# Kernel tuning notes

Hardware: AMD Instinct MI355X
Metric: run time of the kernel (lower is better)

Reference implementation:

```python
import jax, jax.numpy as jnp
import numpy as np

D_ENC = 640  # encoder feature dim


def setup_inputs() -> dict:
    key = jax.random.key(0)
    k1, k2, k3 = jax.random.split(key, 3)
    B, T, U1 = 8, 256, 65  # U1 = maxU + 1
    D_pred = 640
    V = 1024  # num_outputs + 1
    encoder_out = jax.random.normal(k1, (B, T, D_ENC), dtype=jnp.float32)
    predictor_out = jax.random.normal(k2, (B, U1, D_pred), dtype=jnp.float32)
    W = jax.random.normal(k3, (D_ENC + D_pred, V), dtype=jnp.float32) * 0.02
    b = jnp.zeros((V,), dtype=jnp.float32)
    return {"encoder_out": encoder_out, "predictor_out": predictor_out, "W": W, "b": b}


def reference(encoder_out, predictor_out, W, b):
    # Original: tile enc over U+1, tile pred over T, concat on feature dim, Dense.
    # Mathematically identical: split W into encoder/predictor halves and
    # broadcast-add the two projections (avoids the O(T*U*2D) concat buffer).
    We = W[:D_ENC]   # [D_enc, V]
    Wp = W[D_ENC:]   # [D_pred, V]
    enc_proj = jnp.einsum("btd,dv->btv", encoder_out, We)      # [B, T, V]
    pred_proj = jnp.einsum("bud,dv->buv", predictor_out, Wp)   # [B, U+1, V]
    out = enc_proj[:, :, None, :] + pred_proj[:, None, :, :] + b  # [B, T, U+1, V]
    return out
```

## Files before the change

kernel.cpp:

```cpp
#include <hip/hip_runtime.h>

constexpr int B  = 8;
constexpr int T  = 256;
constexpr int U1 = 65;
constexpr int DK = 640;
constexpr int V  = 1024;

constexpr int M_ENC  = B * T;
constexpr int M_PRED = B * U1;

constexpr int NKS  = DK / 32;
constexpr int RT_E = M_ENC / 16;
constexpr int RT_P = 36;
constexpr int CT   = V / 16;

typedef float  f32x4  __attribute__((ext_vector_type(4)));
typedef short  short8 __attribute__((ext_vector_type(8)));
typedef unsigned short u16x4 __attribute__((ext_vector_type(4)));

__device__ __forceinline__ short f2bf(float f) {
    union { float f; unsigned u; } x; x.f = f;
    unsigned r = x.u + 0x7fffu + ((x.u >> 16) & 1u);
    return (short)(r >> 16);
}
__device__ __forceinline__ f32x4 bf4_to_f32(u16x4 s) {
    f32x4 o;
    union { unsigned u; float f; } x;
    x.u = ((unsigned)s[0]) << 16; o[0] = x.f;
    x.u = ((unsigned)s[1]) << 16; o[1] = x.f;
    x.u = ((unsigned)s[2]) << 16; o[2] = x.f;
    x.u = ((unsigned)s[3]) << 16; o[3] = x.f;
    return o;
}

constexpr int NB_AE = RT_E * NKS * 64 / 256;
constexpr int NB_AP = RT_P * NKS * 64 / 256;
constexpr int NB_BE = CT   * NKS * 64 / 256;
constexpr int NB_BP = NB_BE;

__global__ __launch_bounds__(256) void prep_kernel(
    const float* __restrict__ enc, const float* __restrict__ pred,
    const float* __restrict__ W,
    short* __restrict__ Apack_e, short* __restrict__ Apack_p,
    short* __restrict__ Bpack_e, short* __restrict__ Bpack_p)
{
    const int bid = blockIdx.x;
    const int tid = threadIdx.x;

    if (bid < NB_AE) {
        const int chunk = bid * 256 + tid;
        const int l  = chunk & 63;
        const int ks = (chunk >> 6) % NKS;
        const int rt = chunk / (64 * NKS);
        const int row = rt * 16 + (l & 15);
        const float* src = enc + (size_t)row * DK + ks * 32 + (l >> 4) * 8;
        const f32x4 x = *reinterpret_cast<const f32x4*>(src);
        const f32x4 y = *reinterpret_cast<const f32x4*>(src + 4);
        short8 s;
        s[0]=f2bf(x[0]); s[1]=f2bf(x[1]); s[2]=f2bf(x[2]); s[3]=f2bf(x[3]);
        s[4]=f2bf(y[0]); s[5]=f2bf(y[1]); s[6]=f2bf(y[2]); s[7]=f2bf(y[3]);
        *reinterpret_cast<short8*>(Apack_e + (size_t)chunk * 8) = s;
    } else if (bid < NB_AE + NB_AP) {
        const int chunk = (bid - NB_AE) * 256 + tid;
        const int l  = chunk & 63;
        const int ks = (chunk >> 6) % NKS;
        const int rt = chunk / (64 * NKS);
        const int row = rt * 16 + (l & 15);
        short8 s;
        if (row < M_PRED) {
            const float* src = pred + (size_t)row * DK + ks * 32 + (l >> 4) * 8;
            const f32x4 x = *reinterpret_cast<const f32x4*>(src);
            const f32x4 y = *reinterpret_cast<const f32x4*>(src + 4);
            s[0]=f2bf(x[0]); s[1]=f2bf(x[1]); s[2]=f2bf(x[2]); s[3]=f2bf(x[3]);
            s[4]=f2bf(y[0]); s[5]=f2bf(y[1]); s[6]=f2bf(y[2]); s[7]=f2bf(y[3]);
        } else {
            #pragma unroll
            for (int j = 0; j < 8; ++j) s[j] = 0;
        }
        *reinterpret_cast<short8*>(Apack_p + (size_t)chunk * 8) = s;
    } else {
        const bool isE = (bid < NB_AE + NB_AP + NB_BE);
        const int  base = isE ? (NB_AE + NB_AP) : (NB_AE + NB_AP + NB_BE);
        short* Bp = isE ? Bpack_e : Bpack_p;
        const int kofs = isE ? 0 : DK;
        const int chunk = (bid - base) * 256 + tid;
        const int l  = chunk & 63;
        const int ks = (chunk >> 6) % NKS;
        const int ct = chunk / (64 * NKS);
        const int v  = ct * 16 + (l & 15);
        const int k0 = kofs + ks * 32 + (l >> 4) * 8;
        short8 s;
        #pragma unroll
        for (int j = 0; j < 8; ++j)
            s[j] = f2bf(W[(size_t)(k0 + j) * V + v]);
        *reinterpret_cast<short8*>(Bp + (size_t)chunk * 8) = s;
    }
}

constexpr int NB_GE = (M_ENC / 64) * 16;
constexpr int NB_GP = (RT_P / 4) * 16;

__global__ __launch_bounds__(256) void gemm_kernel(
    const short* __restrict__ Apack_e, const short* __restrict__ Apack_p,
    const short* __restrict__ Bpack_e, const short* __restrict__ Bpack_p,
    const float* __restrict__ bias,
    short* __restrict__ enc_proj, short* __restrict__ pred_proj)
{
    const bool isE = (blockIdx.x < NB_GE);
    const int  lb  = isE ? blockIdx.x : blockIdx.x - NB_GE;
    const int  rb  = lb >> 4;
    const int  cb  = lb & 15;

    const short* Ap = isE ? Apack_e : Apack_p;
    const short* Bp = isE ? Bpack_e : Bpack_p;
    short* O        = isE ? enc_proj : pred_proj;
    const int M     = isE ? M_ENC : M_PRED;

    const int wid  = threadIdx.x >> 6;
    const int lane = threadIdx.x & 63;
    const int wr   = wid >> 1, wc = wid & 1;
    const int m    = lane & 15, g = lane >> 4;

    const int rt0 = rb * 4 + wr * 2;
    const int ct0 = cb * 4 + wc * 2;

    const short* a0p = Ap + ((size_t)rt0 * NKS) * 512 + lane * 8;
    const short* a1p = a0p + (size_t)NKS * 512;
    const short* b0p = Bp + ((size_t)ct0 * NKS) * 512 + lane * 8;
    const short* b1p = b0p + (size_t)NKS * 512;

    f32x4 z4; z4[0]=z4[1]=z4[2]=z4[3]=0.f;
    f32x4 acc00 = z4, acc01 = z4, acc10 = z4, acc11 = z4;

    #pragma unroll 4
    for (int ks = 0; ks < NKS; ++ks) {
        const size_t o = (size_t)ks * 512;
        const short8 a0 = *reinterpret_cast<const short8*>(a0p + o);
        const short8 a1 = *reinterpret_cast<const short8*>(a1p + o);
        const short8 b0 = *reinterpret_cast<const short8*>(b0p + o);
        const short8 b1 = *reinterpret_cast<const short8*>(b1p + o);
        acc00 = __builtin_amdgcn_mfma_f32_16x16x32_bf16(a0, b0, acc00, 0, 0, 0);
        acc01 = __builtin_amdgcn_mfma_f32_16x16x32_bf16(a0, b1, acc01, 0, 0, 0);
        acc10 = __builtin_amdgcn_mfma_f32_16x16x32_bf16(a1, b0, acc10, 0, 0, 0);
        acc11 = __builtin_amdgcn_mfma_f32_16x16x32_bf16(a1, b1, acc11, 0, 0, 0);
    }

    #pragma unroll
    for (int nt = 0; nt < 2; ++nt) {
        const int col = (ct0 + nt) * 16 + m;
        const float bv = isE ? 0.f : bias[col];
        #pragma unroll
        for (int mt = 0; mt < 2; ++mt) {
            const f32x4 a = nt ? (mt ? acc11 : acc01) : (mt ? acc10 : acc00);
            #pragma unroll
            for (int q = 0; q < 4; ++q) {
                const int row = (rt0 + mt) * 16 + g * 4 + q;
                if (row < M)
                    O[(size_t)row * V + col] = f2bf(a[q] + bv);
            }
        }
    }
}

__global__ __launch_bounds__(256) void bcast_kernel(
    const short* __restrict__ enc_proj, const short* __restrict__ pred_proj,
    float* __restrict__ out)
{
    const int bt0 = blockIdx.x * 2;
    const int b   = bt0 >> 8;
    const int tid = threadIdx.x;

    const f32x4 e0 = bf4_to_f32(*reinterpret_cast<const u16x4*>(
        enc_proj + (size_t)bt0 * V + tid * 4));
    const f32x4 e1 = bf4_to_f32(*reinterpret_cast<const u16x4*>(
        enc_proj + (size_t)(bt0 + 1) * V + tid * 4));

    const short* p = pred_proj + (size_t)b * U1 * V + tid * 4;
    float* o0 = out + (size_t)bt0 * U1 * V;
    float* o1 = out + (size_t)(bt0 + 1) * U1 * V;

    for (int u0 = 0; u0 < 64; u0 += 8) {
        u16x4 pv[8];
        #pragma unroll
        for (int j = 0; j < 8; ++j)
            pv[j] = *reinterpret_cast<const u16x4*>(p + (size_t)(u0 + j) * V);
        #pragma unroll
        for (int j = 0; j < 8; ++j) {
            const f32x4 pf = bf4_to_f32(pv[j]);
            *(reinterpret_cast<f32x4*>(o0 + (size_t)(u0 + j) * V) + tid) = e0 + pf;
            *(reinterpret_cast<f32x4*>(o1 + (size_t)(u0 + j) * V) + tid) = e1 + pf;
        }
    }
    {
        const f32x4 pf = bf4_to_f32(
            *reinterpret_cast<const u16x4*>(p + (size_t)64 * V));
        *(reinterpret_cast<f32x4*>(o0 + (size_t)64 * V) + tid) = e0 + pf;
        *(reinterpret_cast<f32x4*>(o1 + (size_t)64 * V) + tid) = e1 + pf;
    }
}

extern "C" void kernel_launch(void* const* d_in, const int* in_sizes, int n_in,
                              void* d_out, int out_size, void* d_ws, size_t ws_size,
                              hipStream_t stream)
{
    const float* enc  = (const float*)d_in[0];
    const float* pred = (const float*)d_in[1];
    const float* W    = (const float*)d_in[2];
    const float* bias = (const float*)d_in[3];
    float* out = (float*)d_out;

    short* Apack_e  = (short*)d_ws;
    short* Apack_p  = Apack_e + (size_t)RT_E * NKS * 512;
    short* Bpack_e  = Apack_p + (size_t)RT_P * NKS * 512;
    short* Bpack_p  = Bpack_e + (size_t)CT * NKS * 512;
    short* enc_proj = Bpack_p + (size_t)CT * NKS * 512;
    short* pred_proj = enc_proj + (size_t)M_ENC * V;

    prep_kernel<<<NB_AE + NB_AP + NB_BE + NB_BP, 256, 0, stream>>>(
        enc, pred, W, Apack_e, Apack_p, Bpack_e, Bpack_p);

    gemm_kernel<<<NB_GE + NB_GP, 256, 0, stream>>>(
        Apack_e, Apack_p, Bpack_e, Bpack_p, bias, enc_proj, pred_proj);

    bcast_kernel<<<M_ENC / 2, 256, 0, stream>>>(enc_proj, pred_proj, out);
}
```

Before: 124.4 us.

## Fuse encoder GEMM into broadcast-add kernel using shared-memory tiles

Splits the GEMM so that only the predictor projection runs as its own kernel. The encoder projection is computed inside the broadcast kernel: each block does a 16-row by 128-column MFMA tile, stages the result and the matching predictor slice in LDS, then writes all U+1 output rows. This drops the enc_proj round trip through global memory and one launch. The cost is that 1024 blocks each recompute a small GEMM before streaming roughly 537MB of output, and the narrower 128-column stores and longer per-block serial work may reduce write efficiency.

```diff
diff --git a/kernel.cpp b/kernel.cpp
--- a/kernel.cpp
+++ b/kernel.cpp
@@ -97,24 +97,14 @@
     }
 }
 
-constexpr int NB_GE = (M_ENC / 64) * 16;
 constexpr int NB_GP = (RT_P / 4) * 16;
 
-__global__ __launch_bounds__(256) void gemm_kernel(
-    const short* __restrict__ Apack_e, const short* __restrict__ Apack_p,
-    const short* __restrict__ Bpack_e, const short* __restrict__ Bpack_p,
-    const float* __restrict__ bias,
-    short* __restrict__ enc_proj, short* __restrict__ pred_proj)
-{
-    const bool isE = (blockIdx.x < NB_GE);
-    const int  lb  = isE ? blockIdx.x : blockIdx.x - NB_GE;
-    const int  rb  = lb >> 4;
-    const int  cb  = lb & 15;
-
-    const short* Ap = isE ? Apack_e : Apack_p;
-    const short* Bp = isE ? Bpack_e : Bpack_p;
-    short* O        = isE ? enc_proj : pred_proj;
-    const int M     = isE ? M_ENC : M_PRED;
+__global__ __launch_bounds__(256) void gemm_pred_kernel(
+    const short* __restrict__ Apack_p, const short* __restrict__ Bpack_p,
+    const float* __restrict__ bias, short* __restrict__ pred_proj)
+{
+    const int rb = blockIdx.x >> 4;
+    const int cb = blockIdx.x & 15;
 
     const int wid  = threadIdx.x >> 6;
     const int lane = threadIdx.x & 63;
@@ -124,9 +114,9 @@
     const int rt0 = rb * 4 + wr * 2;
     const int ct0 = cb * 4 + wc * 2;
 
-    const short* a0p = Ap + ((size_t)rt0 * NKS) * 512 + lane * 8;
+    const short* a0p = Apack_p + ((size_t)rt0 * NKS) * 512 + lane * 8;
     const short* a1p = a0p + (size_t)NKS * 512;
-    const short* b0p = Bp + ((size_t)ct0 * NKS) * 512 + lane * 8;
+    const short* b0p = Bpack_p + ((size_t)ct0 * NKS) * 512 + lane * 8;
     const short* b1p = b0p + (size_t)NKS * 512;
 
     f32x4 z4; z4[0]=z4[1]=z4[2]=z4[3]=0.f;
@@ -148,54 +138,88 @@
     #pragma unroll
     for (int nt = 0; nt < 2; ++nt) {
         const int col = (ct0 + nt) * 16 + m;
-        const float bv = isE ? 0.f : bias[col];
+        const float bv = bias[col];
         #pragma unroll
         for (int mt = 0; mt < 2; ++mt) {
             const f32x4 a = nt ? (mt ? acc11 : acc01) : (mt ? acc10 : acc00);
             #pragma unroll
             for (int q = 0; q < 4; ++q) {
                 const int row = (rt0 + mt) * 16 + g * 4 + q;
-                if (row < M)
-                    O[(size_t)row * V + col] = f2bf(a[q] + bv);
+                if (row < M_PRED)
+                    pred_proj[(size_t)row * V + col] = f2bf(a[q] + bv);
             }
         }
     }
 }
 
-__global__ __launch_bounds__(256) void bcast_kernel(
-    const short* __restrict__ enc_proj, const short* __restrict__ pred_proj,
-    float* __restrict__ out)
-{
-    const int bt0 = blockIdx.x * 2;
-    const int b   = bt0 >> 8;
-    const int tid = threadIdx.x;
-
+__global__ __launch_bounds__(256) void fused_kernel(
+    const short* __restrict__ Apack_e, const short* __restrict__ Bpack_e,
+    const short* __restrict__ pred_proj, float* __restrict__ out)
+{
+    __shared__ short p_s[U1 * 128];
+    __shared__ short e_s[16 * 128];
+
+    const int rt   = blockIdx.x >> 3;
+    const int cp   = blockIdx.x & 7;
+    const int b    = rt >> 4;
+    const int col0 = cp * 128;
+    const int tid  = threadIdx.x;
+
+    for (int i = tid; i < U1 * 16; i += 256) {
+        const int u = i >> 4;
+        const int c = (i & 15) * 8;
+        *reinterpret_cast<short8*>(p_s + u * 128 + c) =
+            *reinterpret_cast<const short8*>(
+                pred_proj + ((size_t)(b * U1 + u)) * V + col0 + c);
+    }
+
+    const int wid  = tid >> 6;
+    const int lane = tid & 63;
+    const int m    = lane & 15, g = lane >> 4;
+
+    const short* ap  = Apack_e + ((size_t)rt * NKS) * 512 + lane * 8;
+    const int   ct0  = cp * 8 + wid * 2;
+    const short* b0p = Bpack_e + ((size_t)ct0 * NKS) * 512 + lane * 8;
+    const short* b1p = b0p + (size_t)NKS * 512;
+
+    f32x4 z4; z4[0]=z4[1]=z4[2]=z4[3]=0.f;
+    f32x4 acc0 = z4, acc1 = z4;
+
+    #pragma unroll 4
+    for (int ks = 0; ks < NKS; ++ks) {
+        const size_t o = (size_t)ks * 512;
+        const short8 a  = *reinterpret_cast<const short8*>(ap  + o);
+        const short8 b0 = *reinterpret_cast<const short8*>(b0p + o);
+        const short8 b1 = *reinterpret_cast<const short8*>(b1p + o);
+        acc0 = __builtin_amdgcn_mfma_f32_16x16x32_bf16(a, b0, acc0, 0, 0, 0);
+        acc1 = __builtin_amdgcn_mfma_f32_16x16x32_bf16(a, b1, acc1, 0, 0, 0);
+    }
+
+    #pragma unroll
+    for (int nt = 0; nt < 2; ++nt) {
+        const f32x4 a = nt ? acc1 : acc0;
+        const int col = wid * 32 + nt * 16 + m;
+        #pragma unroll
+        for (int q = 0; q < 4; ++q)
+            e_s[(g * 4 + q) * 128 + col] = f2bf(a[q]);
+    }
+    __syncthreads();
+
+    const int c4 = tid & 31;
+    const int r8 = tid >> 5;
     const f32x4 e0 = bf4_to_f32(*reinterpret_cast<const u16x4*>(
-        enc_proj + (size_t)bt0 * V + tid * 4));
+        e_s + r8 * 128 + c4 * 4));
     const f32x4 e1 = bf4_to_f32(*reinterpret_cast<const u16x4*>(
-        enc_proj + (size_t)(bt0 + 1) * V + tid * 4));
-
-    const short* p = pred_proj + (size_t)b * U1 * V + tid * 4;
-    float* o0 = out + (size_t)bt0 * U1 * V;
-    float* o1 = out + (size_t)(bt0 + 1) * U1 * V;
-
-    for (int u0 = 0; u0 < 64; u0 += 8) {
-        u16x4 pv[8];
-        #pragma unroll
-        for (int j = 0; j < 8; ++j)
-            pv[j] = *reinterpret_cast<const u16x4*>(p + (size_t)(u0 + j) * V);
-        #pragma unroll
-        for (int j = 0; j < 8; ++j) {
-            const f32x4 pf = bf4_to_f32(pv[j]);
-            *(reinterpret_cast<f32x4*>(o0 + (size_t)(u0 + j) * V) + tid) = e0 + pf;
-            *(reinterpret_cast<f32x4*>(o1 + (size_t)(u0 + j) * V) + tid) = e1 + pf;
-        }
-    }
-    {
-        const f32x4 pf = bf4_to_f32(
-            *reinterpret_cast<const u16x4*>(p + (size_t)64 * V));
-        *(reinterpret_cast<f32x4*>(o0 + (size_t)64 * V) + tid) = e0 + pf;
-        *(reinterpret_cast<f32x4*>(o1 + (size_t)64 * V) + tid) = e1 + pf;
+        e_s + (8 + r8) * 128 + c4 * 4));
+
+    float* o0 = out + ((size_t)(rt * 16 + r8) * U1) * V + col0 + c4 * 4;
+    float* o1 = out + ((size_t)(rt * 16 + 8 + r8) * U1) * V + col0 + c4 * 4;
+
+    for (int u = 0; u < U1; ++u) {
+        const f32x4 pf = bf4_to_f32(*reinterpret_cast<const u16x4*>(
+            p_s + u * 128 + c4 * 4));
+        *reinterpret_cast<f32x4*>(o0 + (size_t)u * V) = e0 + pf;
+        *reinterpret_cast<f32x4*>(o1 + (size_t)u * V) = e1 + pf;
     }
 }
 
@@ -213,14 +237,14 @@
     short* Apack_p  = Apack_e + (size_t)RT_E * NKS * 512;
     short* Bpack_e  = Apack_p + (size_t)RT_P * NKS * 512;
     short* Bpack_p  = Bpack_e + (size_t)CT * NKS * 512;
-    short* enc_proj = Bpack_p + (size_t)CT * NKS * 512;
-    short* pred_proj = enc_proj + (size_t)M_ENC * V;
+    short* pred_proj = Bpack_p + (size_t)CT * NKS * 512;
 
     prep_kernel<<<NB_AE + NB_AP + NB_BE + NB_BP, 256, 0, stream>>>(
         enc, pred, W, Apack_e, Apack_p, Bpack_e, Bpack_p);
 
-    gemm_kernel<<<NB_GE + NB_GP, 256, 0, stream>>>(
-        Apack_e, Apack_p, Bpack_e, Bpack_p, bias, enc_proj, pred_proj);
-
-    bcast_kernel<<<M_ENC / 2, 256, 0, stream>>>(enc_proj, pred_proj, out);
-}
+    gemm_pred_kernel<<<NB_GP, 256, 0, stream>>>(
+        Apack_p, Bpack_p, bias, pred_proj);
+
+    fused_kernel<<<RT_E * 8, 256, 0, stream>>>(
+        Apack_e, Bpack_e, pred_proj, out);
+}
```

New measurement: 130.0 us. +4.5%, slower.
